# Kernel optimization log

Hardware: AMD Instinct MI355X
Metric: run time of the kernel (lower is better)

The kernel has to match this reference:

```python
import jax, jax.numpy as jnp
import numpy as np

LN_EPS = 1e-5
FD_EPS = 1e-3   # cfg.fd_eps
MAX_ITER = 2    # cfg.max_iter; early-exit on tol is a host-side .item() check in torch, omitted for jit (fixed iterations)


def _block(w1, b1, w2, b2, g, beta, x):
    # pre-LN MLP residual block: x + W2 @ gelu(W1 @ LN(x))
    mu = jnp.mean(x, axis=-1, keepdims=True)
    var = jnp.var(x, axis=-1, keepdims=True)
    xn = (x - mu) * jax.lax.rsqrt(var + LN_EPS) * g + beta
    h = jax.nn.gelu(xn @ w1 + b1)
    return x + h @ w2 + b2

# apply block_l to state_l for all l at once: (L,B,T,C) -> (L,B,T,C)
_vblock = jax.vmap(_block, in_axes=(0, 0, 0, 0, 0, 0, 0))


def _scan_solve(As, bs):
    # solve x_l = A_l * x_{l-1} + b_l with x_0 = b_0 (A_0 unused), O(log L)
    def combine(e1, e2):
        A1, c1 = e1
        A2, c2 = e2
        return A2 * A1, A2 * c1 + c2
    _, xs = jax.lax.associative_scan(combine, (As, bs), axis=0)
    return xs


def setup_inputs() -> dict:
    key = jax.random.key(0)
    ks = jax.random.split(key, 3)
    L, B, T, C, F = 12, 2, 512, 768, 3072
    return {
        "x0": jax.random.normal(ks[0], (B, T, C), jnp.float32),
        "w1": jax.random.normal(ks[1], (L, C, F), jnp.float32) * 0.02,
        "b1": jnp.zeros((L, F), jnp.float32),
        "w2": jax.random.normal(ks[2], (L, F, C), jnp.float32) * 0.02,
        "b2": jnp.zeros((L, C), jnp.float32),
        "g": jnp.ones((L, C), jnp.float32),
        "beta": jnp.zeros((L, C), jnp.float32),
    }


def reference(x0, w1, b1, w2, b2, g, beta):
    L = w1.shape[0]
    # picard warmstart: states[l+1] = block_l(x0) (computed under torch.no_grad)
    warm = jax.lax.stop_gradient(
        _vblock(w1, b1, w2, b2, g, beta, jnp.broadcast_to(x0, (L,) + x0.shape)))
    states = jnp.concatenate([x0[None], warm], axis=0)  # (L+1, B, T, C)
    key = jax.random.key(42)
    for it in range(MAX_ITER):
        # residuals r_l = block_l(x_l) - x_{l+1}
        outs = _vblock(w1, b1, w2, b2, g, beta, states[:-1])
        res = outs - states[1:]
        # quasi-DEER FD diagonal Jacobian (Rademacher probe, under no_grad)
        sg = jax.lax.stop_gradient(states[:-1])
        v = jnp.sign(jax.random.normal(jax.random.fold_in(key, it), sg.shape, jnp.float32))
        op = _vblock(w1, b1, w2, b2, g, beta, sg + FD_EPS * v)
        om = _vblock(w1, b1, w2, b2, g, beta, sg - FD_EPS * v)
        diag_J = jax.lax.stop_gradient((op - om) / (2.0 * FD_EPS) * v)
        # damping k=0 for quasi-deer -> A_l = diag_J_l, b_l = r_l
        delta = _scan_solve(diag_J, res)  # (L, B, T, C)
        states = states.at[1:].add(delta)
    return states[-1]
```

## Files before the change

### kernel.cpp

```cpp
#include <hip/hip_runtime.h>
#include <hip/hip_bf16.h>
#include <stdint.h>


typedef __bf16 bf16;
typedef __bf16 bf16x8 __attribute__((ext_vector_type(8)));
typedef float f32x4 __attribute__((ext_vector_type(4)));

#define LAY_A   1572864
#define LAY_W   2359296
#define LAY_Z   6291456
#define LAY_S   786432

#define GLDS16(gp, lp) __builtin_amdgcn_global_load_lds(                      \
    (const __attribute__((address_space(1))) void*)(gp),                      \
    (__attribute__((address_space(3))) void*)(lp), 16, 0, 0)

#define WAITVM(N) asm volatile("s_waitcnt vmcnt(%0)" :: "n"(N) : "memory")
#define CFENCE()  asm volatile("" ::: "memory")

#define TF_ROT(x0, x1, n) { x0 += x1; x1 = (x1 << n) | (x1 >> (32 - n)); x1 ^= x0; }
__host__ __device__ __forceinline__ void threefry2x32(
    uint32_t k1, uint32_t k2, uint32_t c0, uint32_t c1, uint32_t& o0, uint32_t& o1)
{
  const uint32_t ks2 = k1 ^ k2 ^ 0x1BD11BDAu;
  uint32_t x0 = c0 + k1, x1 = c1 + k2;
  TF_ROT(x0,x1,13) TF_ROT(x0,x1,15) TF_ROT(x0,x1,26) TF_ROT(x0,x1,6)
  x0 += k2;  x1 += ks2 + 1u;
  TF_ROT(x0,x1,17) TF_ROT(x0,x1,29) TF_ROT(x0,x1,16) TF_ROT(x0,x1,24)
  x0 += ks2; x1 += k1 + 2u;
  TF_ROT(x0,x1,13) TF_ROT(x0,x1,15) TF_ROT(x0,x1,26) TF_ROT(x0,x1,6)
  x0 += k1;  x1 += k2 + 3u;
  TF_ROT(x0,x1,17) TF_ROT(x0,x1,29) TF_ROT(x0,x1,16) TF_ROT(x0,x1,24)
  x0 += k2;  x1 += ks2 + 4u;
  TF_ROT(x0,x1,13) TF_ROT(x0,x1,15) TF_ROT(x0,x1,26) TF_ROT(x0,x1,6)
  x0 += ks2; x1 += k1 + 5u;
  o0 = x0; o1 = x1;
}

__global__ __launch_bounds__(256) void transpose_kernel(
    const float* __restrict__ w, bf16* __restrict__ wt, int R, int Cc)
{
  __shared__ float tile[32][33];
  const int l = blockIdx.z;
  const float* wp = w + (size_t)l * R * Cc;
  bf16* wtp = wt + (size_t)l * R * Cc;
  const int c0 = blockIdx.x * 32;
  const int r0 = blockIdx.y * 32;
  const int tx = threadIdx.x & 31, ty = threadIdx.x >> 5;
  #pragma unroll
  for (int q = 0; q < 4; ++q)
    tile[ty + q * 8][tx] = wp[(size_t)(r0 + ty + q * 8) * Cc + c0 + tx];
  __syncthreads();
  #pragma unroll
  for (int q = 0; q < 4; ++q)
    wtp[(size_t)(c0 + ty + q * 8) * R + r0 + tx] = (bf16)tile[tx][ty + q * 8];
}

__device__ __forceinline__ void gelu2(float z, float& h, float& dg)
{
  const float z2 = z * z;
  const float u = 0.7978845608028654f * (z + 0.044715f * z2 * z);
  const float t = tanhf(u);
  h = 0.5f * z * (1.f + t);
  dg = 0.5f * (1.f + t) +
       0.5f * z * (1.f - t * t) * 0.7978845608028654f * (1.f + 0.134145f * z2);
}

template <int MODE>
__global__ __launch_bounds__(256, 2) void gemm_dbuf(
    const bf16* __restrict__ Abase, const bf16* __restrict__ Bbase,
    bf16* __restrict__ zh_out, float* __restrict__ states,
    float* __restrict__ resA, const bf16* __restrict__ vbuf,
    const float* __restrict__ bias1, const float* __restrict__ b2,
    const float* __restrict__ x0, int Mt)
{
  constexpr int LDAB  = (MODE <= 1) ? 768 : 3072;
  constexpr int NKT   = (MODE <= 1) ? 12 : 48;
  constexpr int NTN   = (MODE <= 1) ? 24 : 6;
  constexpr int ACH   = 16;
  constexpr int BCH   = 16;
  constexpr int NCH   = (ACH + BCH) / 4;
  constexpr int ABYTES = 16384;
  constexpr int TILE  = ABYTES + BCH * 1024;
  constexpr size_t LSA = (MODE <= 1) ? LAY_A : LAY_Z;

  __shared__ __align__(16) char lds[2][TILE];

  const int tid  = threadIdx.x;
  const int lane = tid & 63;
  const int wid  = tid >> 6;
  const int wr   = wid >> 1;
  const int wc   = wid & 1;
  const int r16  = lane & 15;
  const int hi   = lane >> 4;

  const int nwg = gridDim.x;
  const int bid = blockIdx.x;
  const int swz = (bid & 7) * (nwg >> 3) + (bid >> 3);
  const int per_l = Mt * NTN;
  const int l   = swz / per_l;
  const int rr_ = swz - l * per_l;
  const int mt  = rr_ / NTN;
  const int nt  = rr_ - mt * NTN;
  const int m0  = mt * 128, n0 = nt * 128;

  const bf16* A = Abase + (size_t)l * LSA   + (size_t)m0 * LDAB;
  const bf16* B = Bbase + (size_t)l * LAY_W + (size_t)n0 * LDAB;

  const int rsub = lane >> 3;
  const int c8   = (lane & 7) ^ rsub;
  auto STAGE = [&](char* dst, int kt) {
    #pragma unroll
    for (int j = 0; j < NCH; ++j) {
      const int chunk = j * 4 + wid;
      if (chunk < ACH) {
        const int row = chunk * 8 + rsub;
        GLDS16(A + (size_t)row * LDAB + kt + c8 * 8, dst + chunk * 1024);
      } else {
        const int row = (chunk - ACH) * 8 + rsub;
        GLDS16(B + (size_t)row * LDAB + kt + c8 * 8,
               dst + ABYTES + (chunk - ACH) * 1024);
      }
    }
  };

  f32x4 acc[4][4] = {};

  auto COMPUTE = [&](const char* buf) {
    const char* As = buf;
    const char* Bs = buf + ABYTES;
    const int xw = (r16 & 7) << 4;
    #pragma unroll
    for (int kk = 0; kk < 2; ++kk) {
      const int cb = kk * 64;
      bf16x8 bfrag[4];
      #pragma unroll
      for (int ni = 0; ni < 4; ++ni) {
        const int rn = wc * 64 + ni * 16 + r16;
        bfrag[ni] = *(const bf16x8*)(Bs + rn * 128 + ((cb + hi * 16) ^ xw));
      }
      bf16x8 afrag[4];
      #pragma unroll
      for (int q = 0; q < 4; ++q) {
        const int rm = wr * 64 + q * 16 + r16;
        afrag[q] = *(const bf16x8*)(As + rm * 128 + ((cb + hi * 16) ^ xw));
      }
      #pragma unroll
      for (int q = 0; q < 4; ++q)
        #pragma unroll
        for (int ni = 0; ni < 4; ++ni)
          acc[q][ni] = __builtin_amdgcn_mfma_f32_16x16x32_bf16(
              afrag[q], bfrag[ni], acc[q][ni], 0, 0, 0);
    }
  };

  STAGE(lds[0], 0);
  STAGE(lds[1], 64);
  WAITVM(NCH);
  __builtin_amdgcn_s_barrier();
  CFENCE();
  COMPUTE(lds[0]);
  #pragma unroll 1
  for (int t = 1; t < NKT; ++t) {
    CFENCE();
    __builtin_amdgcn_s_barrier();
    CFENCE();
    if (t + 1 < NKT) {
      STAGE(lds[(t + 1) & 1], (t + 1) * 64);
      WAITVM(NCH);
    } else {
      WAITVM(0);
    }
    __builtin_amdgcn_s_barrier();
    CFENCE();
    COMPUTE(lds[t & 1]);
  }

  #pragma unroll
  for (int mi = 0; mi < 4; ++mi) {
    const int row0 = m0 + wr * 64 + mi * 16 + hi * 4;
    #pragma unroll
    for (int ni = 0; ni < 4; ++ni) {
      const int col = n0 + wc * 64 + ni * 16 + r16;
      if (MODE == 0) {
        bf16* Cp = zh_out + (size_t)l * LAY_Z;
        const float bias = bias1[l * 3072 + col];
        #pragma unroll
        for (int r = 0; r < 4; ++r) {
          float h, dg;
          gelu2(acc[mi][ni][r] + bias, h, dg);
          Cp[(size_t)(row0 + r) * 3072 + col] = (bf16)h;
        }
      } else if (MODE == 1) {
        bf16* Cp = zh_out + (size_t)l * LAY_Z;
        const float bias = bias1[l * 3072 + col];
        #pragma unroll
        for (int p = 0; p < 2; ++p) {
          float h, dg;
          gelu2(acc[mi][ni][2 * p] + bias, h, dg);
          Cp[(size_t)(row0 + 2 * p) * 3072 + col] = (bf16)h;
          Cp[(size_t)(row0 + 2 * p + 1) * 3072 + col] =
              (bf16)(dg * acc[mi][ni][2 * p + 1]);
        }
      } else if (MODE == 2) {
        float* Sp = states + (size_t)(l + 1) * LAY_S;
        const float bb = b2[l * 768 + col];
        #pragma unroll
        for (int r = 0; r < 4; ++r)
          Sp[(size_t)(row0 + r) * 768 + col] =
              acc[mi][ni][r] + bb + x0[(size_t)(row0 + r) * 768 + col];
      } else {
        float* Rp = resA + (size_t)l * LAY_A;
        const float bb = b2[l * 768 + col];
        #pragma unroll
        for (int p = 0; p < 2; ++p) {
          const int tok = (row0 >> 1) + p;
          Rp[(size_t)tok * 768 + col] = acc[mi][ni][2 * p] + bb
              + states[(size_t)l * LAY_S + (size_t)tok * 768 + col]
              - states[(size_t)(l + 1) * LAY_S + (size_t)tok * 768 + col];
          const float vv = (float)vbuf[(size_t)l * LAY_S +
                                       (size_t)tok * 768 + col];
          Rp[LAY_S + (size_t)tok * 768 + col] =
              1.0f + acc[mi][ni][2 * p + 1] * vv;
        }
      }
    }
  }
}

__global__ __launch_bounds__(256) void ln_warm_kernel(
    const float* __restrict__ x0, const float* __restrict__ g,
    const float* __restrict__ beta, bf16* __restrict__ a_buf)
{
  const int row = blockIdx.x * 4 + (threadIdx.x >> 6);
  const int lane = threadIdx.x & 63;
  const float* x = x0 + (size_t)row * 768;
  float xl[12];
  float s1 = 0.f, s2 = 0.f;
  #pragma unroll
  for (int j = 0; j < 12; ++j) {
    float t = x[lane + 64 * j];
    xl[j] = t; s1 += t; s2 += t * t;
  }
  #pragma unroll
  for (int off = 1; off < 64; off <<= 1) {
    s1 += __shfl_xor(s1, off);
    s2 += __shfl_xor(s2, off);
  }
  const float mu = s1 * (1.f / 768.f);
  const float var = s2 * (1.f / 768.f) - mu * mu;
  const float rstd = rsqrtf(var + 1e-5f);
  float xh[12];
  #pragma unroll
  for (int j = 0; j < 12; ++j) xh[j] = (xl[j] - mu) * rstd;
  for (int l = 0; l < 12; ++l) {
    const float* gp = g + l * 768;
    const float* bp = beta + l * 768;
    bf16* ap = a_buf + (size_t)l * LAY_A + (size_t)row * 768;
    #pragma unroll
    for (int j = 0; j < 12; ++j) {
      const int c = lane + 64 * j;
      ap[c] = (bf16)(xh[j] * gp[c] + bp[c]);
    }
  }
}

__global__ __launch_bounds__(256) void ln_iter_kernel(
    const float* __restrict__ states, bf16* __restrict__ vbuf,
    const float* __restrict__ g, const float* __restrict__ beta,
    bf16* __restrict__ a_buf, uint32_t k1, uint32_t k2)
{
  const int gr = blockIdx.x * 4 + (threadIdx.x >> 6);
  const int l = gr >> 10;
  const int row = gr & 1023;
  const int lane = threadIdx.x & 63;
  const float* x = states + (size_t)l * LAY_S + (size_t)row * 768;
  bf16* vp = vbuf + (size_t)gr * 768;
  float xl[12], vl[12];
  float s1 = 0.f, s2 = 0.f, sv = 0.f, sxv = 0.f;
  #pragma unroll
  for (int j = 0; j < 12; ++j) {
    const int c = lane + 64 * j;
    const float t = x[c];
    uint32_t o0, o1;
    threefry2x32(k1, k2, 0u, (uint32_t)gr * 768u + (uint32_t)c, o0, o1);
    const float u = ((o0 ^ o1) & 0x80000000u) ? 1.0f : -1.0f;
    vp[c] = (bf16)u;
    xl[j] = t; vl[j] = u;
    s1 += t; s2 += t * t; sv += u; sxv += t * u;
  }
  #pragma unroll
  for (int off = 1; off < 64; off <<= 1) {
    s1 += __shfl_xor(s1, off); s2 += __shfl_xor(s2, off);
    sv += __shfl_xor(sv, off); sxv += __shfl_xor(sxv, off);
  }
  const float mu = s1 * (1.f / 768.f);
  const float var = s2 * (1.f / 768.f) - mu * mu;
  const float rstd = rsqrtf(var + 1e-5f);
  const float mv = sv * (1.f / 768.f);
  const float mhv = rstd * (sxv * (1.f / 768.f) - mu * mv);
  const float* gp = g + l * 768;
  const float* bp = beta + l * 768;
  bf16* ap = a_buf + (size_t)l * LAY_A + (size_t)(2 * row) * 768;
  bf16* dp = ap + 768;
  #pragma unroll
  for (int j = 0; j < 12; ++j) {
    const int c = lane + 64 * j;
    const float xh = (xl[j] - mu) * rstd;
    ap[c] = (bf16)(xh * gp[c] + bp[c]);
    dp[c] = (bf16)(rstd * ((vl[j] - mv) - xh * mhv) * gp[c]);
  }
}

__global__ __launch_bounds__(256) void scan_kernel(
    const float* __restrict__ resA, float* __restrict__ states)
{
  const size_t i = (size_t)blockIdx.x * 256 + threadIdx.x;
  float run = resA[i];
  states[LAY_S + i] += run;
  #pragma unroll
  for (int l = 1; l < 12; ++l) {
    const float b  = resA[(size_t)l * LAY_A + i];
    const float Aa = resA[(size_t)l * LAY_A + LAY_S + i];
    run = b + Aa * run;
    states[(size_t)(l + 1) * LAY_S + i] += run;
  }
}

extern "C" void kernel_launch(void* const* d_in, const int* in_sizes, int n_in,
                              void* d_out, int out_size, void* d_ws, size_t ws_size,
                              hipStream_t stream)
{
  const float* x0   = (const float*)d_in[0];
  const float* w1   = (const float*)d_in[1];
  const float* b1   = (const float*)d_in[2];
  const float* w2   = (const float*)d_in[3];
  const float* b2   = (const float*)d_in[4];
  const float* g    = (const float*)d_in[5];
  const float* beta = (const float*)d_in[6];

  char* ws = (char*)d_ws;
  size_t off = 0;
  auto alloc = [&](size_t bytes) -> void* {
    void* p = ws + off;
    off += (bytes + 255) & ~(size_t)255;
    return p;
  };
  bf16*  w1t    = (bf16*)alloc(2ULL * 12 * LAY_W);
  bf16*  w2t    = (bf16*)alloc(2ULL * 12 * LAY_W);
  float* states = (float*)alloc(4ULL * 13 * LAY_S);
  bf16*  a_buf  = (bf16*)alloc(2ULL * 12 * LAY_A);
  bf16*  zh     = (bf16*)alloc(2ULL * 12 * LAY_Z);
  float* resA   = (float*)alloc(4ULL * 12 * LAY_A);
  bf16*  vbuf   = (bf16*)alloc(2ULL * 12 * LAY_S);

  transpose_kernel<<<dim3(96, 24, 12), 256, 0, stream>>>(w1, w1t, 768, 3072);
  transpose_kernel<<<dim3(24, 96, 12), 256, 0, stream>>>(w2, w2t, 3072, 768);
  hipMemcpyAsync(states, x0, 4ULL * LAY_S, hipMemcpyDeviceToDevice, stream);

  ln_warm_kernel<<<256, 256, 0, stream>>>(x0, g, beta, a_buf);
  gemm_dbuf<0><<<2304, 256, 0, stream>>>(a_buf, w1t, zh, states, resA, vbuf,
                                         b1, b2, x0, 8);
  gemm_dbuf<2><<<576, 256, 0, stream>>>(zh, w2t, nullptr, states, resA, vbuf,
                                        b1, b2, x0, 8);

  for (int it = 0; it < 2; ++it) {
    uint32_t k1, k2;
    threefry2x32(0u, 42u, 0u, (uint32_t)it, k1, k2);
    ln_iter_kernel<<<3072, 256, 0, stream>>>(states, vbuf, g, beta, a_buf,
                                             k1, k2);
    gemm_dbuf<1><<<4608, 256, 0, stream>>>(a_buf, w1t, zh, states, resA, vbuf,
                                           b1, b2, x0, 16);
    gemm_dbuf<3><<<1152, 256, 0, stream>>>(zh, w2t, nullptr, states, resA, vbuf,
                                           b1, b2, x0, 16);
    scan_kernel<<<3072, 256, 0, stream>>>(resA, states);
  }

  hipMemcpyAsync(d_out, states + 12ULL * LAY_S, 4ULL * LAY_S,
                 hipMemcpyDeviceToDevice, stream);
}
```

Before: 1.037 ms.

## Load B fragments directly to registers and halve LDS to raise occupancy

The GEMM kernel no longer stages the B (weight) tile through LDS. Each wave loads its B fragments straight from global memory into registers, double-buffered across two register sets, while A is still staged in LDS via global_load_lds. This halves LDS use per block and raises launch_bounds occupancy from 2 to 3 blocks per CU, with the main loop unrolled by two to alternate buffers. The cost is higher register pressure, and B is now read directly from global/L2 by both waves sharing a column with no LDS reuse, which may raise memory traffic.

```diff
diff --git a/kernel.cpp b/kernel.cpp
--- a/kernel.cpp
+++ b/kernel.cpp
@@ -68,7 +68,7 @@
 }
 
 template <int MODE>
-__global__ __launch_bounds__(256, 2) void gemm_dbuf(
+__global__ __launch_bounds__(256, 3) void gemm_dbuf(
     const bf16* __restrict__ Abase, const bf16* __restrict__ Bbase,
     bf16* __restrict__ zh_out, float* __restrict__ states,
     float* __restrict__ resA, const bf16* __restrict__ vbuf,
@@ -78,14 +78,10 @@
   constexpr int LDAB  = (MODE <= 1) ? 768 : 3072;
   constexpr int NKT   = (MODE <= 1) ? 12 : 48;
   constexpr int NTN   = (MODE <= 1) ? 24 : 6;
-  constexpr int ACH   = 16;
-  constexpr int BCH   = 16;
-  constexpr int NCH   = (ACH + BCH) / 4;
   constexpr int ABYTES = 16384;
-  constexpr int TILE  = ABYTES + BCH * 1024;
   constexpr size_t LSA = (MODE <= 1) ? LAY_A : LAY_Z;
 
-  __shared__ __align__(16) char lds[2][TILE];
+  __shared__ __align__(16) char lds[2][ABYTES];
 
   const int tid  = threadIdx.x;
   const int lane = tid & 63;
@@ -110,36 +106,39 @@
 
   const int rsub = lane >> 3;
   const int c8   = (lane & 7) ^ rsub;
-  auto STAGE = [&](char* dst, int kt) {
-    #pragma unroll
-    for (int j = 0; j < NCH; ++j) {
-      const int chunk = j * 4 + wid;
-      if (chunk < ACH) {
-        const int row = chunk * 8 + rsub;
-        GLDS16(A + (size_t)row * LDAB + kt + c8 * 8, dst + chunk * 1024);
-      } else {
-        const int row = (chunk - ACH) * 8 + rsub;
-        GLDS16(B + (size_t)row * LDAB + kt + c8 * 8,
-               dst + ABYTES + (chunk - ACH) * 1024);
-      }
+
+  const bf16* ag[4];
+  #pragma unroll
+  for (int j = 0; j < 4; ++j)
+    ag[j] = A + (size_t)((j * 4 + wid) * 8 + rsub) * LDAB + c8 * 8;
+  auto STAGEA = [&](char* dst) {
+    #pragma unroll
+    for (int j = 0; j < 4; ++j) {
+      GLDS16(ag[j], dst + (j * 4 + wid) * 1024);
+      ag[j] += 64;
     }
   };
 
+  const bf16* bp[4];
+  #pragma unroll
+  for (int ni = 0; ni < 4; ++ni)
+    bp[ni] = B + (size_t)(wc * 64 + ni * 16 + r16) * LDAB + hi * 8;
+  auto BFLOAD = [&](bf16x8* dst) {
+    #pragma unroll
+    for (int ni = 0; ni < 4; ++ni) {
+      dst[ni]     = *(const bf16x8*)(bp[ni]);
+      dst[4 + ni] = *(const bf16x8*)(bp[ni] + 32);
+      bp[ni] += 64;
+    }
+  };
+
   f32x4 acc[4][4] = {};
-
-  auto COMPUTE = [&](const char* buf) {
-    const char* As = buf;
-    const char* Bs = buf + ABYTES;
-    const int xw = (r16 & 7) << 4;
+  const int xw = (r16 & 7) << 4;
+
+  auto COMPUTE = [&](const char* As, const bf16x8* bfr) {
     #pragma unroll
     for (int kk = 0; kk < 2; ++kk) {
       const int cb = kk * 64;
-      bf16x8 bfrag[4];
-      #pragma unroll
-      for (int ni = 0; ni < 4; ++ni) {
-        const int rn = wc * 64 + ni * 16 + r16;
-        bfrag[ni] = *(const bf16x8*)(Bs + rn * 128 + ((cb + hi * 16) ^ xw));
-      }
       bf16x8 afrag[4];
       #pragma unroll
       for (int q = 0; q < 4; ++q) {
@@ -151,31 +150,47 @@
         #pragma unroll
         for (int ni = 0; ni < 4; ++ni)
           acc[q][ni] = __builtin_amdgcn_mfma_f32_16x16x32_bf16(
-              afrag[q], bfrag[ni], acc[q][ni], 0, 0, 0);
+              afrag[q], bfr[kk * 4 + ni], acc[q][ni], 0, 0, 0);
     }
   };
 
-  STAGE(lds[0], 0);
-  STAGE(lds[1], 64);
-  WAITVM(NCH);
+  bf16x8 bA[8], bB[8];
+  BFLOAD(bA); STAGEA(lds[0]);
+  BFLOAD(bB); STAGEA(lds[1]);
+  WAITVM(12);
   __builtin_amdgcn_s_barrier();
   CFENCE();
-  COMPUTE(lds[0]);
+  COMPUTE(lds[0], bA);
   #pragma unroll 1
-  for (int t = 1; t < NKT; ++t) {
+  for (int tp = 1; tp + 1 < NKT; tp += 2) {
     CFENCE();
     __builtin_amdgcn_s_barrier();
     CFENCE();
-    if (t + 1 < NKT) {
-      STAGE(lds[(t + 1) & 1], (t + 1) * 64);
-      WAITVM(NCH);
+    BFLOAD(bA); STAGEA(lds[0]);
+    WAITVM(12);
+    __builtin_amdgcn_s_barrier();
+    CFENCE();
+    COMPUTE(lds[1], bB);
+    CFENCE();
+    __builtin_amdgcn_s_barrier();
+    CFENCE();
+    if (tp + 2 < NKT) {
+      BFLOAD(bB); STAGEA(lds[1]);
+      WAITVM(12);
     } else {
       WAITVM(0);
     }
     __builtin_amdgcn_s_barrier();
     CFENCE();
-    COMPUTE(lds[t & 1]);
-  }
+    COMPUTE(lds[0], bA);
+  }
+  CFENCE();
+  __builtin_amdgcn_s_barrier();
+  CFENCE();
+  WAITVM(0);
+  __builtin_amdgcn_s_barrier();
+  CFENCE();
+  COMPUTE(lds[1], bB);
 
   #pragma unroll
   for (int mi = 0; mi < 4; ++mi) {
```

Result: slower. 1.564 ms (+50.9%).

## Add 256x256-tile 8-wave GEMM with split-phase pipelining for first MLP matmul

Applied to the files above, without the earlier changes.

Replaces the 128x128 double-buffered GEMM used for the LN(x)@W1 + GELU stage with a new 512-thread kernel computing 256x256 tiles. Each k-step is split into two half-stages, with barriers separating the MFMA phases from the LDS reads and global-to-LDS copies, and setprio raised around the MFMA bursts. The larger tile raises arithmetic intensity and cuts how often the A and W1 tiles are reloaded. In exchange it uses 128 KB of LDS per block, needs more accumulator registers, and launches fewer blocks, which may lower occupancy. The second GEMM keeps the old kernel, now specialised to its two modes only.

```diff
diff --git a/kernel.cpp b/kernel.cpp
--- a/kernel.cpp
+++ b/kernel.cpp
@@ -17,6 +17,7 @@
     (__attribute__((address_space(3))) void*)(lp), 16, 0, 0)
 
 #define WAITVM(N) asm volatile("s_waitcnt vmcnt(%0)" :: "n"(N) : "memory")
+#define LGKM0()   asm volatile("s_waitcnt lgkmcnt(0)" ::: "memory")
 #define CFENCE()  asm volatile("" ::: "memory")
 
 #define TF_ROT(x0, x1, n) { x0 += x1; x1 = (x1 << n) | (x1 >> (32 - n)); x1 ^= x0; }
@@ -68,22 +69,171 @@
 }
 
 template <int MODE>
+__global__ __launch_bounds__(512, 2) void gemm1_8p(
+    const bf16* __restrict__ Abase, const bf16* __restrict__ Bbase,
+    bf16* __restrict__ zh_out, const float* __restrict__ bias1, int Mt)
+{
+  constexpr int LDAB = 768;
+  constexpr int NKT  = 12;
+  constexpr int NTN  = 12;
+  constexpr int HB   = 32768;
+
+  __shared__ __align__(16) char lds[2][2 * HB];
+
+  const int tid  = threadIdx.x;
+  const int lane = tid & 63;
+  const int wid  = tid >> 6;
+  const int wr   = wid >> 2;
+  const int wc   = wid & 3;
+  const int r16  = lane & 15;
+  const int hi   = lane >> 4;
+
+  const int nwg = gridDim.x;
+  const int bid = blockIdx.x;
+  const int swz = (bid & 7) * (nwg >> 3) + (bid >> 3);
+  const int per_l = Mt * NTN;
+  const int l   = swz / per_l;
+  const int rr_ = swz - l * per_l;
+  const int mt  = rr_ / NTN;
+  const int nt  = rr_ - mt * NTN;
+  const int m0  = mt * 256, n0 = nt * 256;
+
+  const bf16* A = Abase + (size_t)l * LAY_A + (size_t)m0 * LDAB;
+  const bf16* B = Bbase + (size_t)l * LAY_W + (size_t)n0 * LDAB;
+
+  const int rsub = lane >> 3;
+  const int c8   = (lane & 7) ^ rsub;
+  const bf16* ag[4];
+  const bf16* bg[4];
+  #pragma unroll
+  for (int j = 0; j < 4; ++j) {
+    const int chunk = j * 8 + wid;
+    ag[j] = A + (size_t)(chunk * 8 + rsub) * LDAB + c8 * 8;
+    bg[j] = B + (size_t)(chunk * 8 + rsub) * LDAB + c8 * 8;
+  }
+  auto SHALF0 = [&](char* buf) {
+    #pragma unroll
+    for (int j = 0; j < 2; ++j) {
+      GLDS16(ag[j], buf + (j * 8 + wid) * 1024);
+      GLDS16(bg[j], buf + HB + (j * 8 + wid) * 1024);
+    }
+  };
+  auto SHALF1 = [&](char* buf) {
+    #pragma unroll
+    for (int j = 2; j < 4; ++j) {
+      GLDS16(ag[j], buf + (j * 8 + wid) * 1024);
+      GLDS16(bg[j], buf + HB + (j * 8 + wid) * 1024);
+    }
+    #pragma unroll
+    for (int j = 0; j < 4; ++j) { ag[j] += 64; bg[j] += 64; }
+  };
+
+  f32x4 acc[8][4] = {};
+  bf16x8 bfr[4], af[4];
+  const int xw = (r16 & 7) << 4;
+
+  auto DSB = [&](const char* buf, int kk) {
+    const char* Bs = buf + HB;
+    #pragma unroll
+    for (int ni = 0; ni < 4; ++ni) {
+      const int rn = wc * 64 + ni * 16 + r16;
+      bfr[ni] = *(const bf16x8*)(Bs + rn * 128 + ((kk * 64 + hi * 16) ^ xw));
+    }
+  };
+  auto DSA = [&](const char* buf, int mh, int kk) {
+    #pragma unroll
+    for (int q = 0; q < 4; ++q) {
+      const int rm = wr * 128 + (mh * 4 + q) * 16 + r16;
+      af[q] = *(const bf16x8*)(buf + rm * 128 + ((kk * 64 + hi * 16) ^ xw));
+    }
+  };
+  auto MF = [&](int mh) {
+    __builtin_amdgcn_s_setprio(1);
+    #pragma unroll
+    for (int q = 0; q < 4; ++q)
+      #pragma unroll
+      for (int ni = 0; ni < 4; ++ni)
+        acc[mh * 4 + q][ni] = __builtin_amdgcn_mfma_f32_16x16x32_bf16(
+            af[q], bfr[ni], acc[mh * 4 + q][ni], 0, 0, 0);
+    __builtin_amdgcn_s_setprio(0);
+  };
+
+  SHALF0(lds[0]);
+  SHALF1(lds[0]);
+  WAITVM(0);
+  __builtin_amdgcn_s_barrier();
+  CFENCE();
+
+  #pragma unroll 1
+  for (int t = 0; t < NKT; ++t) {
+    char* cur = lds[t & 1];
+    char* nxt = lds[(t & 1) ^ 1];
+    const bool more = (t + 1 < NKT);
+    DSB(cur, 0); DSA(cur, 0, 0);
+    if (more) SHALF0(nxt);
+    CFENCE(); __builtin_amdgcn_s_barrier(); LGKM0();
+    MF(0);
+    CFENCE(); __builtin_amdgcn_s_barrier(); CFENCE();
+    DSA(cur, 1, 0);
+    if (more) SHALF1(nxt);
+    CFENCE(); __builtin_amdgcn_s_barrier(); LGKM0();
+    MF(1);
+    CFENCE(); __builtin_amdgcn_s_barrier(); CFENCE();
+    DSB(cur, 1); DSA(cur, 0, 1);
+    CFENCE(); __builtin_amdgcn_s_barrier(); LGKM0();
+    MF(0);
+    CFENCE(); __builtin_amdgcn_s_barrier(); CFENCE();
+    DSA(cur, 1, 1);
+    CFENCE(); __builtin_amdgcn_s_barrier(); LGKM0();
+    MF(1);
+    if (more) {
+      WAITVM(0);
+      CFENCE(); __builtin_amdgcn_s_barrier(); CFENCE();
+    }
+  }
+
+  bf16* Cp = zh_out + (size_t)l * LAY_Z;
+  #pragma unroll
+  for (int mi = 0; mi < 8; ++mi) {
+    const int row0 = m0 + wr * 128 + mi * 16 + hi * 4;
+    #pragma unroll
+    for (int ni = 0; ni < 4; ++ni) {
+      const int col = n0 + wc * 64 + ni * 16 + r16;
+      const float bias = bias1[l * 3072 + col];
+      if (MODE == 0) {
+        #pragma unroll
+        for (int r = 0; r < 4; ++r) {
+          float h, dg;
+          gelu2(acc[mi][ni][r] + bias, h, dg);
+          Cp[(size_t)(row0 + r) * 3072 + col] = (bf16)h;
+        }
+      } else {
+        #pragma unroll
+        for (int p = 0; p < 2; ++p) {
+          float h, dg;
+          gelu2(acc[mi][ni][2 * p] + bias, h, dg);
+          Cp[(size_t)(row0 + 2 * p) * 3072 + col] = (bf16)h;
+          Cp[(size_t)(row0 + 2 * p + 1) * 3072 + col] =
+              (bf16)(dg * acc[mi][ni][2 * p + 1]);
+        }
+      }
+    }
+  }
+}
+
+template <int MODE>
 __global__ __launch_bounds__(256, 2) void gemm_dbuf(
     const bf16* __restrict__ Abase, const bf16* __restrict__ Bbase,
-    bf16* __restrict__ zh_out, float* __restrict__ states,
-    float* __restrict__ resA, const bf16* __restrict__ vbuf,
-    const float* __restrict__ bias1, const float* __restrict__ b2,
+    float* __restrict__ states, float* __restrict__ resA,
+    const bf16* __restrict__ vbuf, const float* __restrict__ b2,
     const float* __restrict__ x0, int Mt)
 {
-  constexpr int LDAB  = (MODE <= 1) ? 768 : 3072;
-  constexpr int NKT   = (MODE <= 1) ? 12 : 48;
-  constexpr int NTN   = (MODE <= 1) ? 24 : 6;
-  constexpr int ACH   = 16;
-  constexpr int BCH   = 16;
-  constexpr int NCH   = (ACH + BCH) / 4;
+  constexpr int LDAB  = 3072;
+  constexpr int NKT   = 48;
+  constexpr int NTN   = 6;
+  constexpr int NCH   = 8;
   constexpr int ABYTES = 16384;
-  constexpr int TILE  = ABYTES + BCH * 1024;
-  constexpr size_t LSA = (MODE <= 1) ? LAY_A : LAY_Z;
+  constexpr int TILE  = ABYTES + 16384;
 
   __shared__ __align__(16) char lds[2][TILE];
 
@@ -105,7 +255,7 @@
   const int nt  = rr_ - mt * NTN;
   const int m0  = mt * 128, n0 = nt * 128;
 
-  const bf16* A = Abase + (size_t)l * LSA   + (size_t)m0 * LDAB;
+  const bf16* A = Abase + (size_t)l * LAY_Z + (size_t)m0 * LDAB;
   const bf16* B = Bbase + (size_t)l * LAY_W + (size_t)n0 * LDAB;
 
   const int rsub = lane >> 3;
@@ -114,13 +264,13 @@
     #pragma unroll
     for (int j = 0; j < NCH; ++j) {
       const int chunk = j * 4 + wid;
-      if (chunk < ACH) {
+      if (chunk < 16) {
         const int row = chunk * 8 + rsub;
         GLDS16(A + (size_t)row * LDAB + kt + c8 * 8, dst + chunk * 1024);
       } else {
-        const int row = (chunk - ACH) * 8 + rsub;
+        const int row = (chunk - 16) * 8 + rsub;
         GLDS16(B + (size_t)row * LDAB + kt + c8 * 8,
-               dst + ABYTES + (chunk - ACH) * 1024);
+               dst + ABYTES + (chunk - 16) * 1024);
       }
     }
   };
@@ -183,36 +333,15 @@
     #pragma unroll
     for (int ni = 0; ni < 4; ++ni) {
       const int col = n0 + wc * 64 + ni * 16 + r16;
-      if (MODE == 0) {
-        bf16* Cp = zh_out + (size_t)l * LAY_Z;
-        const float bias = bias1[l * 3072 + col];
-        #pragma unroll
-        for (int r = 0; r < 4; ++r) {
-          float h, dg;
-          gelu2(acc[mi][ni][r] + bias, h, dg);
-          Cp[(size_t)(row0 + r) * 3072 + col] = (bf16)h;
-        }
-      } else if (MODE == 1) {
-        bf16* Cp = zh_out + (size_t)l * LAY_Z;
-        const float bias = bias1[l * 3072 + col];
-        #pragma unroll
-        for (int p = 0; p < 2; ++p) {
-          float h, dg;
-          gelu2(acc[mi][ni][2 * p] + bias, h, dg);
-          Cp[(size_t)(row0 + 2 * p) * 3072 + col] = (bf16)h;
-          Cp[(size_t)(row0 + 2 * p + 1) * 3072 + col] =
-              (bf16)(dg * acc[mi][ni][2 * p + 1]);
-        }
-      } else if (MODE == 2) {
+      const float bb = b2[l * 768 + col];
+      if (MODE == 2) {
         float* Sp = states + (size_t)(l + 1) * LAY_S;
-        const float bb = b2[l * 768 + col];
         #pragma unroll
         for (int r = 0; r < 4; ++r)
           Sp[(size_t)(row0 + r) * 768 + col] =
               acc[mi][ni][r] + bb + x0[(size_t)(row0 + r) * 768 + col];
       } else {
         float* Rp = resA + (size_t)l * LAY_A;
-        const float bb = b2[l * 768 + col];
         #pragma unroll
         for (int p = 0; p < 2; ++p) {
           const int tok = (row0 >> 1) + p;
@@ -360,20 +489,17 @@
   hipMemcpyAsync(states, x0, 4ULL * LAY_S, hipMemcpyDeviceToDevice, stream);
 
   ln_warm_kernel<<<256, 256, 0, stream>>>(x0, g, beta, a_buf);
-  gemm_dbuf<0><<<2304, 256, 0, stream>>>(a_buf, w1t, zh, states, resA, vbuf,
-                                         b1, b2, x0, 8);
-  gemm_dbuf<2><<<576, 256, 0, stream>>>(zh, w2t, nullptr, states, resA, vbuf,
-                                        b1, b2, x0, 8);
+  gemm1_8p<0><<<576, 512, 0, stream>>>(a_buf, w1t, zh, b1, 4);
+  gemm_dbuf<2><<<576, 256, 0, stream>>>(zh, w2t, states, resA, vbuf, b2, x0, 8);
 
   for (int it = 0; it < 2; ++it) {
     uint32_t k1, k2;
     threefry2x32(0u, 42u, 0u, (uint32_t)it, k1, k2);
     ln_iter_kernel<<<3072, 256, 0, stream>>>(states, vbuf, g, beta, a_buf,
                                              k1, k2);
-    gemm_dbuf<1><<<4608, 256, 0, stream>>>(a_buf, w1t, zh, states, resA, vbuf,
-                                           b1, b2, x0, 16);
-    gemm_dbuf<3><<<1152, 256, 0, stream>>>(zh, w2t, nullptr, states, resA, vbuf,
-                                           b1, b2, x0, 16);
+    gemm1_8p<1><<<1152, 512, 0, stream>>>(a_buf, w1t, zh, b1, 8);
+    gemm_dbuf<3><<<1152, 256, 0, stream>>>(zh, w2t, states, resA, vbuf, b2,
+                                           x0, 16);
     scan_kernel<<<3072, 256, 0, stream>>>(resA, states);
   }
 
```

Result: no change. 1.052 ms (+1.5%).
